# Performance work log

Hardware: AMD Instinct MI355X
Metric: run time of the kernel (lower is better)

Reference implementation:

```python
import jax, jax.numpy as jnp
import numpy as np

N, H, HEADS, E = 4096, 256, 4, 262144
DH = H // HEADS
EPS = 1e-5


def _ln(x, g, b):
    mu = jnp.mean(x, axis=-1, keepdims=True)
    var = jnp.mean(jnp.square(x - mu), axis=-1, keepdims=True)
    return (x - mu) / jnp.sqrt(var + EPS) * g + b


def setup_inputs() -> dict:
    key = jax.random.key(0)
    ks = jax.random.split(key, 20)
    s = 0.02
    inp = {
        "h": jax.random.normal(ks[0], (N, H), jnp.float32),
        "edge_index": jax.random.randint(ks[1], (2, E), 0, N, jnp.int64 if jax.config.read("jax_enable_x64") else jnp.int32),
        "W_src": jax.random.normal(ks[2], (H, H), jnp.float32) * s,
        "b_src": jnp.zeros((H,), jnp.float32),
        "W_tgt": jax.random.normal(ks[3], (H, H), jnp.float32) * s,
        "b_tgt": jnp.zeros((H,), jnp.float32),
        "Wq": jax.random.normal(ks[4], (H, H), jnp.float32) * s,
        "bq": jnp.zeros((H,), jnp.float32),
        "Wk": jax.random.normal(ks[5], (H, H), jnp.float32) * s,
        "bk": jnp.zeros((H,), jnp.float32),
        "Wv": jax.random.normal(ks[6], (H, H), jnp.float32) * s,
        "bv": jnp.zeros((H,), jnp.float32),
        "Wo": jax.random.normal(ks[7], (H, H), jnp.float32) * s,
        "bo": jnp.zeros((H,), jnp.float32),
        "W1": jax.random.normal(ks[8], (H, 2 * H), jnp.float32) * s,
        "b1": jnp.zeros((2 * H,), jnp.float32),
        "W2": jax.random.normal(ks[9], (2 * H, H), jnp.float32) * s,
        "b2": jnp.zeros((H,), jnp.float32),
        "g1": jnp.ones((H,), jnp.float32),
        "be1": jnp.zeros((H,), jnp.float32),
        "g2": jnp.ones((H,), jnp.float32),
        "be2": jnp.zeros((H,), jnp.float32),
    }
    return inp


def reference(h, edge_index, W_src, b_src, W_tgt, b_tgt, Wq, bq, Wk, bk, Wv, bv,
              Wo, bo, W1, b1, W2, b2, g1, be1, g2, be2):
    src, dst = edge_index[0], edge_index[1]
    # gather + linear + add per edge: (E, H)
    edge_emb = (h[src] @ W_src + b_src) + (h[dst] @ W_tgt + b_tgt)
    # scatter-add to target nodes, normalize by in-degree (clamped at 1)
    agg = jax.ops.segment_sum(edge_emb, dst, num_segments=N)
    deg = jax.ops.segment_sum(jnp.ones((E,), h.dtype), dst, num_segments=N)
    agg = agg / jnp.maximum(deg, 1.0)[:, None]
    # multi-head attention: queries = h, keys/values = agg (batch=1, seq=N)
    q = (h @ Wq + bq).reshape(N, HEADS, DH)
    k = (agg @ Wk + bk).reshape(N, HEADS, DH)
    v = (agg @ Wv + bv).reshape(N, HEADS, DH)
    scores = jnp.einsum("nhd,mhd->hnm", q, k) / jnp.sqrt(jnp.asarray(DH, h.dtype))
    attn = jax.nn.softmax(scores, axis=-1)
    ctx = jnp.einsum("hnm,mhd->nhd", attn, v).reshape(N, H)
    attn_out = ctx @ Wo + bo
    # residual + LN (dropout is identity in eval mode)
    x = _ln(h + attn_out, g1, be1)
    ffn = jax.nn.gelu(x @ W1 + b1, approximate=False) @ W2 + b2
    return _ln(x + ffn, g2, be2)
```

## Files before the change

### kernel.cpp

```cpp
#include <hip/hip_runtime.h>

#define N_NODES 4096
#define HID 256
#define N_EDGES 262144
#define N_HEADS 4
#define DHEAD 64

typedef unsigned short u16;
typedef unsigned long long u64;
typedef __attribute__((ext_vector_type(8))) short bf16x8;
typedef __attribute__((ext_vector_type(4))) float f32x4;

__device__ __forceinline__ float b2f(u16 u) {
  union { unsigned int i; float f; } c; c.i = ((unsigned int)u) << 16; return c.f;
}
__device__ __forceinline__ u16 f2b(float f) {
  union { float f; unsigned int i; } c; c.f = f;
  unsigned int x = c.i;
  unsigned int r = (x + 0x7fffu + ((x >> 16) & 1u)) >> 16;
  return (u16)r;
}
__device__ __forceinline__ u16 f2b_trunc(float f) {
  union { float f; unsigned int i; } c; c.f = f;
  return (u16)(c.i >> 16);
}

struct PrepArgs {
  const void* wsrc[8]; u16* wdst[8]; int wR[8]; int wC[8]; int wboff[8];
  const void* bs[12]; u16* bd[12]; int bn[12];
};
__global__ __launch_bounds__(256) void k_prep(
    const void* __restrict__ h_r, u16* __restrict__ h_c, PrepArgs P,
    const unsigned* __restrict__ g1raw, const unsigned* __restrict__ eiraw,
    const int* __restrict__ ei, int* __restrict__ cnt, int* __restrict__ flags) {
  __shared__ u16 t[32][33];
  int b = blockIdx.x, tid = threadIdx.x;
  int f = (g1raw[0] == 0x3F800000u) ? 1 : 0;
  if (b < 1024) {
    int gi = b * 256 + tid;
    if (f) {
      float4 v = ((const float4*)h_r)[gi];
      u64 pk = (u64)f2b(v.x) | ((u64)f2b(v.y) << 16) |
               ((u64)f2b(v.z) << 32) | ((u64)f2b(v.w) << 48);
      ((u64*)h_c)[gi] = pk;
    } else {
      ((uint2*)h_c)[gi] = ((const uint2*)h_r)[gi];
    }
  } else if (b < 1664) {
    int rb = b - 1024;
    int jj = 0;
#pragma unroll
    for (int i2 = 1; i2 < 8; i2++) jj = (rb >= P.wboff[i2]) ? i2 : jj;
    int local = rb - P.wboff[jj];
    int C = P.wC[jj], R = P.wR[jj];
    int nbx = C / 32;
    int c0 = (local % nbx) * 32, r0 = (local / nbx) * 32;
    int tx = tid & 31, ty = tid >> 5;
    const void* src = P.wsrc[jj];
    u16* dst = P.wdst[jj];
    for (int i = ty; i < 32; i += 8) {
      size_t idx = (size_t)(r0 + i) * C + c0 + tx;
      t[i][tx] = f ? f2b(((const float*)src)[idx]) : ((const u16*)src)[idx];
    }
    __syncthreads();
    for (int i = ty; i < 32; i += 8)
      dst[(size_t)(c0 + i) * R + r0 + tx] = t[tx][i];
  } else if (b == 1664) {
    if (tid == 0) {
      unsigned any = 0;
      for (int i = 0; i < 64; i++) any |= eiraw[2 * i + 1];
      flags[0] = f;
      flags[1] = (any == 0u) ? 1 : 0;
    }
    for (int j = 0; j < 12; j++)
      for (int i = tid; i < P.bn[j]; i += 256)
        P.bd[j][i] = f ? f2b(((const float*)P.bs[j])[i]) : ((const u16*)P.bs[j])[i];
  } else {
    unsigned hi = eiraw[2 * (tid & 63) + 1];
#pragma unroll
    for (int m2 = 1; m2 <= 32; m2 <<= 1) hi |= __shfl_xor(hi, m2, 64);
    int i64 = (hi == 0u);
    int e = (b - 1665) * 256 + tid;
    int d = i64 ? ei[2 * (N_EDGES + e)] : ei[N_EDGES + e];
    atomicAdd(&cnt[d], 1);
  }
}

__global__ void k_scan(const int* __restrict__ cnt, int* __restrict__ row_start,
                       int* __restrict__ cursor) {
  __shared__ int part[256];
  int t = threadIdx.x;
  int loc[16];
  int s = 0;
#pragma unroll
  for (int i = 0; i < 16; i++) { loc[i] = s; s += cnt[t * 16 + i]; }
  part[t] = s;
  __syncthreads();
  for (int ofs = 1; ofs < 256; ofs <<= 1) {
    int v = (t >= ofs) ? part[t - ofs] : 0;
    __syncthreads();
    part[t] += v;
    __syncthreads();
  }
  int excl = part[t] - s;
#pragma unroll
  for (int i = 0; i < 16; i++) {
    int v = excl + loc[i];
    row_start[t * 16 + i] = v;
    cursor[t * 16 + i] = v;
  }
  if (t == 255) row_start[N_NODES] = part[255];
}

__global__ void k_fill(const int* __restrict__ ei, int* __restrict__ cursor,
                       int* __restrict__ eidx, const unsigned* __restrict__ eiraw) {
  int tid = threadIdx.x;
  unsigned hi = eiraw[2 * (tid & 63) + 1];
#pragma unroll
  for (int m2 = 1; m2 <= 32; m2 <<= 1) hi |= __shfl_xor(hi, m2, 64);
  int i64 = (hi == 0u);
  int e = blockIdx.x * 256 + tid;
  int d = i64 ? ei[2 * (N_EDGES + e)] : ei[N_EDGES + e];
  int s = i64 ? ei[2 * e] : ei[e];
  int pos = atomicAdd(&cursor[d], 1);
  eidx[pos] = s;
}

__global__ __launch_bounds__(256) void k_gather(
    const int* __restrict__ row_start, const int* __restrict__ eidx,
    const u16* __restrict__ hs, const u16* __restrict__ ht,
    u16* __restrict__ aggb) {
  int n = blockIdx.x, t = threadIdx.x;
  int beg = row_start[n], end = row_start[n + 1];
  float acc = 0.f;
  int j = beg;
  for (; j + 3 < end; j += 4) {
    int s0 = eidx[j], s1 = eidx[j + 1], s2 = eidx[j + 2], s3 = eidx[j + 3];
    acc += b2f(hs[(size_t)s0 * HID + t]);
    acc += b2f(hs[(size_t)s1 * HID + t]);
    acc += b2f(hs[(size_t)s2 * HID + t]);
    acc += b2f(hs[(size_t)s3 * HID + t]);
  }
  for (; j < end; j++) acc += b2f(hs[(size_t)eidx[j] * HID + t]);
  float dg = (float)(end - beg);
  float a = (acc + dg * b2f(ht[(size_t)n * HID + t])) / fmaxf(dg, 1.f);
  aggb[(size_t)n * HID + t] = f2b(a);
}

struct GemmOuts { void* p[3]; int mode[3]; float scale[3]; };
template <int GELU>
__global__ __launch_bounds__(256) void k_gemm_bt(
    const u16* __restrict__ A, const u16* __restrict__ Bt,
    const u16* __restrict__ bias, GemmOuts outs, int ncol, int K) {
  __shared__ u16 As[64][72];
  __shared__ u16 Bs[64][72];
  int tid = threadIdx.x;
  int wave = tid >> 6, lane = tid & 63;
  int ln = lane & 15, quad = lane >> 4;
  int m0 = blockIdx.y * 64, n0 = blockIdx.x * 64;
  int wm = (wave >> 1) * 32, wn = (wave & 1) * 32;
  int srow = tid >> 2, scol = (tid & 3) * 16;
  const u16* pA = &A[(size_t)(m0 + srow) * K + scol];
  const u16* pB = &Bt[(size_t)(n0 + srow) * K + scol];
  f32x4 acc[2][2] = {};
  for (int k0 = 0; k0 < K; k0 += 64) {
    uint4 va0 = *(const uint4*)(pA + k0);
    uint4 va1 = *(const uint4*)(pA + k0 + 8);
    uint4 vb0 = *(const uint4*)(pB + k0);
    uint4 vb1 = *(const uint4*)(pB + k0 + 8);
    __syncthreads();
    *(uint4*)&As[srow][scol] = va0; *(uint4*)&As[srow][scol + 8] = va1;
    *(uint4*)&Bs[srow][scol] = vb0; *(uint4*)&Bs[srow][scol + 8] = vb1;
    __syncthreads();
#pragma unroll
    for (int s2 = 0; s2 < 2; s2++) {
      bf16x8 a0 = *(const bf16x8*)&As[wm + ln][s2 * 32 + quad * 8];
      bf16x8 a1 = *(const bf16x8*)&As[wm + 16 + ln][s2 * 32 + quad * 8];
      bf16x8 b0 = *(const bf16x8*)&Bs[wn + ln][s2 * 32 + quad * 8];
      bf16x8 b1 = *(const bf16x8*)&Bs[wn + 16 + ln][s2 * 32 + quad * 8];
      acc[0][0] = __builtin_amdgcn_mfma_f32_16x16x32_bf16(a0, b0, acc[0][0], 0, 0, 0);
      acc[0][1] = __builtin_amdgcn_mfma_f32_16x16x32_bf16(a0, b1, acc[0][1], 0, 0, 0);
      acc[1][0] = __builtin_amdgcn_mfma_f32_16x16x32_bf16(a1, b0, acc[1][0], 0, 0, 0);
      acc[1][1] = __builtin_amdgcn_mfma_f32_16x16x32_bf16(a1, b1, acc[1][1], 0, 0, 0);
    }
  }
  int which = n0 / ncol;
  int nloc0 = n0 - which * ncol;
  int md = outs.mode[which];
  float sc = outs.scale[which];
#pragma unroll
  for (int t = 0; t < 2; t++)
#pragma unroll
    for (int u = 0; u < 2; u++) {
      int lc = nloc0 + wn + u * 16 + ln;
      float bb = b2f(bias[n0 + wn + u * 16 + ln]);
      float c4[4];
#pragma unroll
      for (int r = 0; r < 4; r++) {
        float c = (acc[t][u][r] + bb) * sc;
        if (GELU) c = 0.5f * c * (1.0f + erff(c * 0.70710678118654752f));
        c4[r] = c;
      }
      int gm0 = m0 + wm + t * 16 + quad * 4;
      if (md == 0) {
        u16* dp = (u16*)outs.p[which];
#pragma unroll
        for (int r = 0; r < 4; r++) dp[(size_t)(gm0 + r) * ncol + lc] = f2b(c4[r]);
      } else if (md == 1) {
        float* dp = (float*)outs.p[which];
#pragma unroll
        for (int r = 0; r < 4; r++) dp[(size_t)(gm0 + r) * ncol + lc] = c4[r];
      } else {
        u64 pk = (u64)f2b(c4[0]) | ((u64)f2b(c4[1]) << 16) |
                 ((u64)f2b(c4[2]) << 32) | ((u64)f2b(c4[3]) << 48);
        *(u64*)&((u16*)outs.p[which])[(size_t)lc * 4096 + gm0] = pk;
      }
    }
}

struct PoPtrs { u16* p[8]; };
struct PoCPtrs { const u16* p[8]; };
__global__ __launch_bounds__(256) void k_attn_split(
    const u16* __restrict__ q, const u16* __restrict__ k,
    const u16* __restrict__ vt, PoPtrs pw, float* __restrict__ lout, int S) {
  __shared__ u16 ks[64][72];
  __shared__ u16 vs[64][72];
  __shared__ u16 ps[4][16][72];
  int tid = threadIdx.x;
  int wv = tid >> 6, lane = tid & 63, ln = lane & 15, quad = lane >> 4;
  int hh = blockIdx.y, q0 = blockIdx.x * 64, bz = blockIdx.z;
  int kchunk = N_NODES / S;
  int kbeg = bz * kchunk, kend = kbeg + kchunk;
  const u16* qrow = &q[(size_t)(q0 + wv * 16 + ln) * HID + hh * DHEAD];
  bf16x8 aq0 = *(const bf16x8*)&qrow[quad * 8];
  bf16x8 aq1 = *(const bf16x8*)&qrow[32 + quad * 8];
  f32x4 o[4] = {};
  float l_r[4] = {0.f, 0.f, 0.f, 0.f};
  int srow = tid >> 2, scol = (tid & 3) * 16;
  const u16* kbase = &k[(size_t)srow * HID + hh * DHEAD + scol];
  const u16* vbase = &vt[(size_t)(hh * DHEAD + srow) * N_NODES + scol];

  for (int k0 = kbeg; k0 < kend; k0 += 64) {
    *(uint4*)&ks[srow][scol]     = *(const uint4*)(kbase + (size_t)k0 * HID);
    *(uint4*)&ks[srow][scol + 8] = *(const uint4*)(kbase + (size_t)k0 * HID + 8);
    *(uint4*)&vs[srow][scol]     = *(const uint4*)(vbase + k0);
    *(uint4*)&vs[srow][scol + 8] = *(const uint4*)(vbase + k0 + 8);
    __syncthreads();

    f32x4 s[4];
#pragma unroll
    for (int u = 0; u < 4; u++) {
      bf16x8 b0 = *(const bf16x8*)&ks[u * 16 + ln][quad * 8];
      bf16x8 b1 = *(const bf16x8*)&ks[u * 16 + ln][32 + quad * 8];
      f32x4 z = {};
      z = __builtin_amdgcn_mfma_f32_16x16x32_bf16(aq0, b0, z, 0, 0, 0);
      s[u] = __builtin_amdgcn_mfma_f32_16x16x32_bf16(aq1, b1, z, 0, 0, 0);
    }
#pragma unroll
    for (int u = 0; u < 4; u++)
#pragma unroll
      for (int r = 0; r < 4; r++) {
        float p = __expf(s[u][r]);
        l_r[r] += p;
        ps[wv][quad * 4 + r][u * 16 + ln] = f2b_trunc(p);
      }
    __syncthreads();

    bf16x8 ap0 = *(const bf16x8*)&ps[wv][ln][quad * 8];
    bf16x8 ap1 = *(const bf16x8*)&ps[wv][ln][32 + quad * 8];
#pragma unroll
    for (int u = 0; u < 4; u++) {
      bf16x8 bv0 = *(const bf16x8*)&vs[u * 16 + ln][quad * 8];
      bf16x8 bv1 = *(const bf16x8*)&vs[u * 16 + ln][32 + quad * 8];
      o[u] = __builtin_amdgcn_mfma_f32_16x16x32_bf16(ap0, bv0, o[u], 0, 0, 0);
      o[u] = __builtin_amdgcn_mfma_f32_16x16x32_bf16(ap1, bv1, o[u], 0, 0, 0);
    }
    __syncthreads();
  }
  u16* po = pw.p[bz];
#pragma unroll
  for (int u = 0; u < 4; u++)
#pragma unroll
    for (int r = 0; r < 4; r++) {
      int row = q0 + wv * 16 + quad * 4 + r;
      po[((size_t)hh * N_NODES + row) * DHEAD + u * 16 + ln] = f2b(o[u][r]);
    }
#pragma unroll
  for (int mask = 1; mask <= 8; mask <<= 1)
#pragma unroll
    for (int r = 0; r < 4; r++) l_r[r] += __shfl_xor(l_r[r], mask, 64);
  if (ln == 0) {
#pragma unroll
    for (int r = 0; r < 4; r++) {
      int row = q0 + wv * 16 + quad * 4 + r;
      lout[(size_t)(bz * N_HEADS + hh) * N_NODES + row] = l_r[r];
    }
  }
}

__global__ __launch_bounds__(256) void k_attn_combine(
    PoCPtrs pp, const float* __restrict__ lsum, u16* __restrict__ ctx, int S) {
  int t = threadIdx.x;
  int d = t & 63, qq = t >> 6;
  int qrow = blockIdx.x * 4 + qq;
  for (int h = 0; h < N_HEADS; h++) {
    float L = 0.f, o = 0.f;
    for (int s = 0; s < S; s++) {
      L += lsum[(size_t)(s * N_HEADS + h) * N_NODES + qrow];
      o += b2f(pp.p[s][((size_t)h * N_NODES + qrow) * DHEAD + d]);
    }
    ctx[(size_t)qrow * HID + h * DHEAD + d] = f2b(o / L);
  }
}

template <int FINAL>
__global__ __launch_bounds__(256) void k_ln(
    const u16* __restrict__ a, const float* __restrict__ b,
    const u16* __restrict__ g, const u16* __restrict__ be,
    void* __restrict__ out, const int* __restrict__ flags) {
  int tid = threadIdx.x, wv = tid >> 6, lane = tid & 63;
  int row = blockIdx.x * 4 + wv;
  size_t base = (size_t)row * HID + lane * 4;
  uint2 av = *(const uint2*)&a[base];
  float4 bv4 = *(const float4*)&b[base];
  float v[4];
  v[0] = b2f((u16)(av.x & 0xffff)) + bv4.x;
  v[1] = b2f((u16)(av.x >> 16)) + bv4.y;
  v[2] = b2f((u16)(av.y & 0xffff)) + bv4.z;
  v[3] = b2f((u16)(av.y >> 16)) + bv4.w;
  float sum = v[0] + v[1] + v[2] + v[3];
#pragma unroll
  for (int mask = 1; mask <= 32; mask <<= 1) sum += __shfl_xor(sum, mask, 64);
  float mu = sum * (1.0f / HID);
  float d[4], sq = 0.f;
#pragma unroll
  for (int i = 0; i < 4; i++) { d[i] = v[i] - mu; sq += d[i] * d[i]; }
#pragma unroll
  for (int mask = 1; mask <= 32; mask <<= 1) sq += __shfl_xor(sq, mask, 64);
  float rstd = rsqrtf(sq * (1.0f / HID) + 1e-5f);
  uint2 gv = *(const uint2*)&g[lane * 4];
  uint2 bev = *(const uint2*)&be[lane * 4];
  float res[4];
  res[0] = d[0] * rstd * b2f((u16)(gv.x & 0xffff)) + b2f((u16)(bev.x & 0xffff));
  res[1] = d[1] * rstd * b2f((u16)(gv.x >> 16)) + b2f((u16)(bev.x >> 16));
  res[2] = d[2] * rstd * b2f((u16)(gv.y & 0xffff)) + b2f((u16)(bev.y & 0xffff));
  res[3] = d[3] * rstd * b2f((u16)(gv.y >> 16)) + b2f((u16)(bev.y >> 16));
#pragma unroll
  for (int i = 0; i < 4; i++)
    if (!(fabsf(res[i]) < 1e30f)) res[i] = FINAL ? 1000.0f : 300.0f;
  if (FINAL && flags[0]) {
    *(float4*)&((float*)out)[base] = make_float4(res[0], res[1], res[2], res[3]);
  } else {
    u64 pk = (u64)f2b(res[0]) | ((u64)f2b(res[1]) << 16) |
             ((u64)f2b(res[2]) << 32) | ((u64)f2b(res[3]) << 48);
    *(u64*)&((u16*)out)[base] = pk;
  }
}

extern "C" void kernel_launch(void* const* d_in, const int* in_sizes, int n_in,
                              void* d_out, int out_size, void* d_ws, size_t ws_size,
                              hipStream_t stream) {
  (void)in_sizes; (void)n_in; (void)out_size;
  const void* h_r    = d_in[0];
  const int*  ei     = (const int*)d_in[1];
  const void* W_r[8] = {d_in[2], d_in[4], d_in[6], d_in[8], d_in[10], d_in[12], d_in[14], d_in[16]};
  const void* b_r[12] = {d_in[3], d_in[5], d_in[7], d_in[9], d_in[11], d_in[13],
                         d_in[15], d_in[17], d_in[18], d_in[19], d_in[20], d_in[21]};

  char* w = (char*)d_ws;
  const size_t MB = 1024 * 1024;
  u16* bufA = (u16*)(w + 0 * MB);
  u16* bufC = (u16*)(w + 2 * MB);
  u16* bufE = (u16*)(w + 4 * MB);
  u16* bufF = (u16*)(w + 6 * MB);
  u16* bufB = (u16*)(w + 8 * MB);
  u16* bufD = (u16*)(w + 10 * MB);
  u16* h_c  = (u16*)(w + 12 * MB);
  size_t off = 14 * MB;
  auto alloc = [&](size_t bytes) -> void* {
    void* p = (void*)(w + off);
    off += (bytes + 255) & ~(size_t)255;
    return p;
  };
  u16* WsrcT = (u16*)alloc((size_t)HID * HID * 2);
  u16* WtgtT = (u16*)alloc((size_t)HID * HID * 2);
  u16* WqT   = (u16*)alloc((size_t)HID * HID * 2);
  u16* WkT   = (u16*)alloc((size_t)HID * HID * 2);
  u16* WvT   = (u16*)alloc((size_t)HID * HID * 2);
  u16* WoT   = (u16*)alloc((size_t)HID * HID * 2);
  u16* W1T   = (u16*)alloc((size_t)HID * 2 * HID * 2);
  u16* W2T   = (u16*)alloc((size_t)HID * 2 * HID * 2);
  u16* bsrc = (u16*)alloc(512); u16* btgt = (u16*)alloc(512);
  u16* bq   = (u16*)alloc(512); u16* bk   = (u16*)alloc(512);
  u16* bv   = (u16*)alloc(512); u16* bo   = (u16*)alloc(512);
  u16* b1   = (u16*)alloc(1024); u16* b2  = (u16*)alloc(512);
  u16* g1   = (u16*)alloc(512); u16* be1  = (u16*)alloc(512);
  u16* g2   = (u16*)alloc(512); u16* be2  = (u16*)alloc(512);
  int* flags = (int*)alloc(256);
  int* cnt  = (int*)alloc((size_t)N_NODES * 4);
  int* rsrt = (int*)alloc((size_t)(N_NODES + 1) * 4);
  int* cur  = (int*)alloc((size_t)N_NODES * 4);
  int* eidx = (int*)alloc((size_t)N_EDGES * 4);

  u16* hs = bufA;  u16* ht = bufB;  u16* qb = bufC;
  u16* aggb = bufD; u16* kb = bufE; u16* vt = bufB;
  u16* ctxb = bufA; u16* xb = bufD;
  float* attn_out = (float*)bufE;
  u16* ffn1 = bufE;
  float* yf = (float*)bufA;
  float* lsum = (float*)eidx;

  int S = 2;
  PoPtrs pw{}; PoCPtrs pc{};
  pw.p[0] = bufF; pw.p[1] = bufD;
  if (ws_size >= off + 12 * MB + 64) {
    S = 8;
    for (int i = 2; i < 8; i++) pw.p[i] = (u16*)(w + off + (size_t)(i - 2) * 2 * MB);
  } else if (ws_size >= off + 4 * MB + 64) {
    S = 4;
    pw.p[2] = (u16*)(w + off);
    pw.p[3] = (u16*)(w + off + 2 * MB);
  }
  for (int i = 0; i < 8; i++) pc.p[i] = pw.p[i];

  hipMemsetAsync(cnt, 0, (size_t)N_NODES * 4, stream);
  PrepArgs P;
  u16* Wdsts[8] = {WsrcT, WtgtT, WqT, WkT, WvT, WoT, W1T, W2T};
  int WR[8] = {HID, HID, HID, HID, HID, HID, HID, 2 * HID};
  int WC[8] = {HID, HID, HID, HID, HID, HID, 2 * HID, HID};
  int boff = 0;
  for (int i = 0; i < 8; i++) {
    P.wsrc[i] = W_r[i]; P.wdst[i] = Wdsts[i]; P.wR[i] = WR[i]; P.wC[i] = WC[i];
    P.wboff[i] = boff;
    boff += (WR[i] / 32) * (WC[i] / 32);
  }
  u16* bdsts[12] = {bsrc, btgt, bq, bk, bv, bo, b1, b2, g1, be1, g2, be2};
  int bns[12] = {256, 256, 256, 256, 256, 256, 512, 256, 256, 256, 256, 256};
  for (int i = 0; i < 12; i++) { P.bs[i] = b_r[i]; P.bd[i] = bdsts[i]; P.bn[i] = bns[i]; }
  k_prep<<<2689, 256, 0, stream>>>(h_r, h_c, P, (const unsigned*)d_in[18],
                                   (const unsigned*)ei, ei, cnt, flags);
  k_scan<<<1, 256, 0, stream>>>(cnt, rsrt, cur);
  k_fill<<<N_EDGES / 256, 256, 0, stream>>>(ei, cur, eidx, (const unsigned*)ei);

  {
    GemmOuts go;
    go.p[0] = hs; go.p[1] = ht; go.p[2] = qb;
    go.mode[0] = 0; go.mode[1] = 0; go.mode[2] = 0;
    go.scale[0] = 1.f; go.scale[1] = 1.f; go.scale[2] = 0.125f;
    k_gemm_bt<0><<<dim3(12, 64), 256, 0, stream>>>(h_c, WsrcT, bsrc, go, HID, HID);
  }
  k_gather<<<N_NODES, 256, 0, stream>>>(rsrt, eidx, hs, ht, aggb);

  {
    GemmOuts go;
    go.p[0] = kb; go.p[1] = vt; go.p[2] = nullptr;
    go.mode[0] = 0; go.mode[1] = 2; go.mode[2] = 0;
    go.scale[0] = 1.f; go.scale[1] = 1.f; go.scale[2] = 1.f;
    k_gemm_bt<0><<<dim3(8, 64), 256, 0, stream>>>(aggb, WkT, bk, go, HID, HID);
  }

  k_attn_split<<<dim3(N_NODES / 64, N_HEADS, S), 256, 0, stream>>>(qb, kb, vt, pw, lsum, S);
  k_attn_combine<<<N_NODES / 4, 256, 0, stream>>>(pc, lsum, ctxb, S);

  {
    GemmOuts go;
    go.p[0] = attn_out; go.p[1] = nullptr; go.p[2] = nullptr;
    go.mode[0] = 1; go.mode[1] = 0; go.mode[2] = 0;
    go.scale[0] = 1.f; go.scale[1] = 1.f; go.scale[2] = 1.f;
    k_gemm_bt<0><<<dim3(4, 64), 256, 0, stream>>>(ctxb, WoT, bo, go, HID, HID);
  }
  k_ln<0><<<N_NODES / 4, 256, 0, stream>>>(h_c, attn_out, g1, be1, xb, flags);

  {
    GemmOuts go;
    go.p[0] = ffn1; go.p[1] = nullptr; go.p[2] = nullptr;
    go.mode[0] = 0; go.mode[1] = 0; go.mode[2] = 0;
    go.scale[0] = 1.f; go.scale[1] = 1.f; go.scale[2] = 1.f;
    k_gemm_bt<1><<<dim3(8, 64), 256, 0, stream>>>(xb, W1T, b1, go, 2 * HID, HID);
  }
  {
    GemmOuts go;
    go.p[0] = yf; go.p[1] = nullptr; go.p[2] = nullptr;
    go.mode[0] = 1; go.mode[1] = 0; go.mode[2] = 0;
    go.scale[0] = 1.f; go.scale[1] = 1.f; go.scale[2] = 1.f;
    k_gemm_bt<0><<<dim3(4, 64), 256, 0, stream>>>(ffn1, W2T, b2, go, HID, 2 * HID);
  }
  k_ln<1><<<N_NODES / 4, 256, 0, stream>>>(xb, yf, g2, be2, d_out, flags);
}
```

Before: 257.6 us.

## Drop LDS staging in GEMMs and software-pipeline attention with MFMA row sums

The GEMM kernel now loads MFMA operands straight from global memory with a compile-time K and unrolled loop, removing the LDS staging and its barriers. The split attention kernel prefetches the next K/V tile into registers while computing the current one. It computes softmax row sums with an MFMA against a ones vector instead of scalar accumulation and shuffles. It also swaps __expf for exp2 by folding log2(e) into the Q scale. The risks are that direct global loads lose reuse across waves and depend on cache hits, and that the row sum is now taken over bf16-truncated probabilities.

```diff
diff --git a/kernel.cpp b/kernel.cpp
--- a/kernel.cpp
+++ b/kernel.cpp
@@ -148,52 +148,42 @@
 }
 
 struct GemmOuts { void* p[3]; int mode[3]; float scale[3]; };
-template <int GELU>
-__global__ __launch_bounds__(256) void k_gemm_bt(
+template <int GELU, int K>
+__global__ __launch_bounds__(256) void k_gemm_nl(
     const u16* __restrict__ A, const u16* __restrict__ Bt,
-    const u16* __restrict__ bias, GemmOuts outs, int ncol, int K) {
-  __shared__ u16 As[64][72];
-  __shared__ u16 Bs[64][72];
+    const u16* __restrict__ bias, GemmOuts outs, int ncol) {
   int tid = threadIdx.x;
   int wave = tid >> 6, lane = tid & 63;
   int ln = lane & 15, quad = lane >> 4;
-  int m0 = blockIdx.y * 64, n0 = blockIdx.x * 64;
-  int wm = (wave >> 1) * 32, wn = (wave & 1) * 32;
-  int srow = tid >> 2, scol = (tid & 3) * 16;
-  const u16* pA = &A[(size_t)(m0 + srow) * K + scol];
-  const u16* pB = &Bt[(size_t)(n0 + srow) * K + scol];
+  int m0 = blockIdx.y * 64 + (wave >> 1) * 32;
+  int n0 = blockIdx.x * 64 + (wave & 1) * 32;
+  const u16* pA0 = &A[(size_t)(m0 + ln) * K + quad * 8];
+  const u16* pA1 = &A[(size_t)(m0 + 16 + ln) * K + quad * 8];
+  const u16* pB0 = &Bt[(size_t)(n0 + ln) * K + quad * 8];
+  const u16* pB1 = &Bt[(size_t)(n0 + 16 + ln) * K + quad * 8];
   f32x4 acc[2][2] = {};
-  for (int k0 = 0; k0 < K; k0 += 64) {
-    uint4 va0 = *(const uint4*)(pA + k0);
-    uint4 va1 = *(const uint4*)(pA + k0 + 8);
-    uint4 vb0 = *(const uint4*)(pB + k0);
-    uint4 vb1 = *(const uint4*)(pB + k0 + 8);
-    __syncthreads();
-    *(uint4*)&As[srow][scol] = va0; *(uint4*)&As[srow][scol + 8] = va1;
-    *(uint4*)&Bs[srow][scol] = vb0; *(uint4*)&Bs[srow][scol + 8] = vb1;
-    __syncthreads();
-#pragma unroll
-    for (int s2 = 0; s2 < 2; s2++) {
-      bf16x8 a0 = *(const bf16x8*)&As[wm + ln][s2 * 32 + quad * 8];
-      bf16x8 a1 = *(const bf16x8*)&As[wm + 16 + ln][s2 * 32 + quad * 8];
-      bf16x8 b0 = *(const bf16x8*)&Bs[wn + ln][s2 * 32 + quad * 8];
-      bf16x8 b1 = *(const bf16x8*)&Bs[wn + 16 + ln][s2 * 32 + quad * 8];
-      acc[0][0] = __builtin_amdgcn_mfma_f32_16x16x32_bf16(a0, b0, acc[0][0], 0, 0, 0);
-      acc[0][1] = __builtin_amdgcn_mfma_f32_16x16x32_bf16(a0, b1, acc[0][1], 0, 0, 0);
-      acc[1][0] = __builtin_amdgcn_mfma_f32_16x16x32_bf16(a1, b0, acc[1][0], 0, 0, 0);
-      acc[1][1] = __builtin_amdgcn_mfma_f32_16x16x32_bf16(a1, b1, acc[1][1], 0, 0, 0);
-    }
-  }
-  int which = n0 / ncol;
-  int nloc0 = n0 - which * ncol;
+#pragma unroll 4
+  for (int k0 = 0; k0 < K; k0 += 32) {
+    bf16x8 a0 = *(const bf16x8*)(pA0 + k0);
+    bf16x8 a1 = *(const bf16x8*)(pA1 + k0);
+    bf16x8 b0 = *(const bf16x8*)(pB0 + k0);
+    bf16x8 b1 = *(const bf16x8*)(pB1 + k0);
+    acc[0][0] = __builtin_amdgcn_mfma_f32_16x16x32_bf16(a0, b0, acc[0][0], 0, 0, 0);
+    acc[0][1] = __builtin_amdgcn_mfma_f32_16x16x32_bf16(a0, b1, acc[0][1], 0, 0, 0);
+    acc[1][0] = __builtin_amdgcn_mfma_f32_16x16x32_bf16(a1, b0, acc[1][0], 0, 0, 0);
+    acc[1][1] = __builtin_amdgcn_mfma_f32_16x16x32_bf16(a1, b1, acc[1][1], 0, 0, 0);
+  }
+  int nblk = blockIdx.x * 64;
+  int which = nblk / ncol;
   int md = outs.mode[which];
   float sc = outs.scale[which];
 #pragma unroll
   for (int t = 0; t < 2; t++)
 #pragma unroll
     for (int u = 0; u < 2; u++) {
-      int lc = nloc0 + wn + u * 16 + ln;
-      float bb = b2f(bias[n0 + wn + u * 16 + ln]);
+      int gn = n0 + u * 16 + ln;
+      int lc = gn - which * ncol;
+      float bb = b2f(bias[gn]);
       float c4[4];
 #pragma unroll
       for (int r = 0; r < 4; r++) {
@@ -201,7 +191,7 @@
         if (GELU) c = 0.5f * c * (1.0f + erff(c * 0.70710678118654752f));
         c4[r] = c;
       }
-      int gm0 = m0 + wm + t * 16 + quad * 4;
+      int gm0 = m0 + t * 16 + quad * 4;
       if (md == 0) {
         u16* dp = (u16*)outs.p[which];
 #pragma unroll
@@ -234,19 +224,30 @@
   const u16* qrow = &q[(size_t)(q0 + wv * 16 + ln) * HID + hh * DHEAD];
   bf16x8 aq0 = *(const bf16x8*)&qrow[quad * 8];
   bf16x8 aq1 = *(const bf16x8*)&qrow[32 + quad * 8];
+  bf16x8 ones;
+#pragma unroll
+  for (int i = 0; i < 8; i++) ones[i] = (short)0x3F80;
   f32x4 o[4] = {};
-  float l_r[4] = {0.f, 0.f, 0.f, 0.f};
+  f32x4 ol = {};
   int srow = tid >> 2, scol = (tid & 3) * 16;
   const u16* kbase = &k[(size_t)srow * HID + hh * DHEAD + scol];
   const u16* vbase = &vt[(size_t)(hh * DHEAD + srow) * N_NODES + scol];
 
+  *(uint4*)&ks[srow][scol]     = *(const uint4*)(kbase + (size_t)kbeg * HID);
+  *(uint4*)&ks[srow][scol + 8] = *(const uint4*)(kbase + (size_t)kbeg * HID + 8);
+  *(uint4*)&vs[srow][scol]     = *(const uint4*)(vbase + kbeg);
+  *(uint4*)&vs[srow][scol + 8] = *(const uint4*)(vbase + kbeg + 8);
+  __syncthreads();
+
   for (int k0 = kbeg; k0 < kend; k0 += 64) {
-    *(uint4*)&ks[srow][scol]     = *(const uint4*)(kbase + (size_t)k0 * HID);
-    *(uint4*)&ks[srow][scol + 8] = *(const uint4*)(kbase + (size_t)k0 * HID + 8);
-    *(uint4*)&vs[srow][scol]     = *(const uint4*)(vbase + k0);
-    *(uint4*)&vs[srow][scol + 8] = *(const uint4*)(vbase + k0 + 8);
-    __syncthreads();
-
+    bool more = (k0 + 64 < kend);
+    uint4 ka0, ka1, va0, va1;
+    if (more) {
+      ka0 = *(const uint4*)(kbase + (size_t)(k0 + 64) * HID);
+      ka1 = *(const uint4*)(kbase + (size_t)(k0 + 64) * HID + 8);
+      va0 = *(const uint4*)(vbase + k0 + 64);
+      va1 = *(const uint4*)(vbase + k0 + 72);
+    }
     f32x4 s[4];
 #pragma unroll
     for (int u = 0; u < 4; u++) {
@@ -259,13 +260,11 @@
 #pragma unroll
     for (int u = 0; u < 4; u++)
 #pragma unroll
-      for (int r = 0; r < 4; r++) {
-        float p = __expf(s[u][r]);
-        l_r[r] += p;
-        ps[wv][quad * 4 + r][u * 16 + ln] = f2b_trunc(p);
-      }
-    __syncthreads();
-
+      for (int r = 0; r < 4; r++)
+        ps[wv][quad * 4 + r][u * 16 + ln] = f2b_trunc(__builtin_amdgcn_exp2f(s[u][r]));
+    __builtin_amdgcn_sched_barrier(0);
+    __builtin_amdgcn_s_waitcnt(0xC07F);
+    __builtin_amdgcn_sched_barrier(0);
     bf16x8 ap0 = *(const bf16x8*)&ps[wv][ln][quad * 8];
     bf16x8 ap1 = *(const bf16x8*)&ps[wv][ln][32 + quad * 8];
 #pragma unroll
@@ -275,6 +274,15 @@
       o[u] = __builtin_amdgcn_mfma_f32_16x16x32_bf16(ap0, bv0, o[u], 0, 0, 0);
       o[u] = __builtin_amdgcn_mfma_f32_16x16x32_bf16(ap1, bv1, o[u], 0, 0, 0);
     }
+    ol = __builtin_amdgcn_mfma_f32_16x16x32_bf16(ap0, ones, ol, 0, 0, 0);
+    ol = __builtin_amdgcn_mfma_f32_16x16x32_bf16(ap1, ones, ol, 0, 0, 0);
+    __syncthreads();
+    if (more) {
+      *(uint4*)&ks[srow][scol]     = ka0;
+      *(uint4*)&ks[srow][scol + 8] = ka1;
+      *(uint4*)&vs[srow][scol]     = va0;
+      *(uint4*)&vs[srow][scol + 8] = va1;
+    }
     __syncthreads();
   }
   u16* po = pw.p[bz];
@@ -285,15 +293,11 @@
       int row = q0 + wv * 16 + quad * 4 + r;
       po[((size_t)hh * N_NODES + row) * DHEAD + u * 16 + ln] = f2b(o[u][r]);
     }
-#pragma unroll
-  for (int mask = 1; mask <= 8; mask <<= 1)
-#pragma unroll
-    for (int r = 0; r < 4; r++) l_r[r] += __shfl_xor(l_r[r], mask, 64);
   if (ln == 0) {
 #pragma unroll
     for (int r = 0; r < 4; r++) {
       int row = q0 + wv * 16 + quad * 4 + r;
-      lout[(size_t)(bz * N_HEADS + hh) * N_NODES + row] = l_r[r];
+      lout[(size_t)(bz * N_HEADS + hh) * N_NODES + row] = ol[r];
     }
   }
 }
@@ -446,8 +450,8 @@
     GemmOuts go;
     go.p[0] = hs; go.p[1] = ht; go.p[2] = qb;
     go.mode[0] = 0; go.mode[1] = 0; go.mode[2] = 0;
-    go.scale[0] = 1.f; go.scale[1] = 1.f; go.scale[2] = 0.125f;
-    k_gemm_bt<0><<<dim3(12, 64), 256, 0, stream>>>(h_c, WsrcT, bsrc, go, HID, HID);
+    go.scale[0] = 1.f; go.scale[1] = 1.f; go.scale[2] = 0.180336880f;
+    k_gemm_nl<0, 256><<<dim3(12, 64), 256, 0, stream>>>(h_c, WsrcT, bsrc, go, HID);
   }
   k_gather<<<N_NODES, 256, 0, stream>>>(rsrt, eidx, hs, ht, aggb);
 
@@ -456,7 +460,7 @@
     go.p[0] = kb; go.p[1] = vt; go.p[2] = nullptr;
     go.mode[0] = 0; go.mode[1] = 2; go.mode[2] = 0;
     go.scale[0] = 1.f; go.scale[1] = 1.f; go.scale[2] = 1.f;
-    k_gemm_bt<0><<<dim3(8, 64), 256, 0, stream>>>(aggb, WkT, bk, go, HID, HID);
+    k_gemm_nl<0, 256><<<dim3(8, 64), 256, 0, stream>>>(aggb, WkT, bk, go, HID);
   }
 
   k_attn_split<<<dim3(N_NODES / 64, N_HEADS, S), 256, 0, stream>>>(qb, kb, vt, pw, lsum, S);
@@ -467,7 +471,7 @@
     go.p[0] = attn_out; go.p[1] = nullptr; go.p[2] = nullptr;
     go.mode[0] = 1; go.mode[1] = 0; go.mode[2] = 0;
     go.scale[0] = 1.f; go.scale[1] = 1.f; go.scale[2] = 1.f;
-    k_gemm_bt<0><<<dim3(4, 64), 256, 0, stream>>>(ctxb, WoT, bo, go, HID, HID);
+    k_gemm_nl<0, 256><<<dim3(4, 64), 256, 0, stream>>>(ctxb, WoT, bo, go, HID);
   }
   k_ln<0><<<N_NODES / 4, 256, 0, stream>>>(h_c, attn_out, g1, be1, xb, flags);
 
@@ -476,14 +480,14 @@
     go.p[0] = ffn1; go.p[1] = nullptr; go.p[2] = nullptr;
     go.mode[0] = 0; go.mode[1] = 0; go.mode[2] = 0;
     go.scale[0] = 1.f; go.scale[1] = 1.f; go.scale[2] = 1.f;
-    k_gemm_bt<1><<<dim3(8, 64), 256, 0, stream>>>(xb, W1T, b1, go, 2 * HID, HID);
+    k_gemm_nl<1, 256><<<dim3(8, 64), 256, 0, stream>>>(xb, W1T, b1, go, 2 * HID);
   }
   {
     GemmOuts go;
     go.p[0] = yf; go.p[1] = nullptr; go.p[2] = nullptr;
     go.mode[0] = 1; go.mode[1] = 0; go.mode[2] = 0;
     go.scale[0] = 1.f; go.scale[1] = 1.f; go.scale[2] = 1.f;
-    k_gemm_bt<0><<<dim3(4, 64), 256, 0, stream>>>(ffn1, W2T, b2, go, HID, 2 * HID);
+    k_gemm_nl<0, 512><<<dim3(4, 64), 256, 0, stream>>>(ffn1, W2T, b2, go, HID);
   }
   k_ln<1><<<N_NODES / 4, 256, 0, stream>>>(xb, yf, g2, be2, d_out, flags);
 }
```

Result: slower. 275.8 us (+7.1%).

## Prefetch next K/V tile in registers, use exp2 and MFMA row sums

Applied to the files above, without the earlier changes.

The attention split kernel now loads the next K/V tile into registers while the current tile is being computed, which overlaps global load latency with MFMA work. The softmax exponent becomes a native exp2, with log2(e) folded into the Q scale, so the separate multiply in expf goes away. Row sums of P are computed by an MFMA against a ones vector instead of per-lane adds plus a shuffle reduction, and the P sum now uses the bf16-truncated values. One barrier is removed inside the wave-private P section, but an extra barrier is added before the shared-memory store, and register pressure rises from the prefetch buffers.

```diff
diff --git a/kernel.cpp b/kernel.cpp
--- a/kernel.cpp
+++ b/kernel.cpp
@@ -234,19 +234,30 @@
   const u16* qrow = &q[(size_t)(q0 + wv * 16 + ln) * HID + hh * DHEAD];
   bf16x8 aq0 = *(const bf16x8*)&qrow[quad * 8];
   bf16x8 aq1 = *(const bf16x8*)&qrow[32 + quad * 8];
+  bf16x8 ones;
+#pragma unroll
+  for (int i = 0; i < 8; i++) ones[i] = (short)0x3F80;
   f32x4 o[4] = {};
-  float l_r[4] = {0.f, 0.f, 0.f, 0.f};
+  f32x4 ol = {};
   int srow = tid >> 2, scol = (tid & 3) * 16;
   const u16* kbase = &k[(size_t)srow * HID + hh * DHEAD + scol];
   const u16* vbase = &vt[(size_t)(hh * DHEAD + srow) * N_NODES + scol];
 
+  *(uint4*)&ks[srow][scol]     = *(const uint4*)(kbase + (size_t)kbeg * HID);
+  *(uint4*)&ks[srow][scol + 8] = *(const uint4*)(kbase + (size_t)kbeg * HID + 8);
+  *(uint4*)&vs[srow][scol]     = *(const uint4*)(vbase + kbeg);
+  *(uint4*)&vs[srow][scol + 8] = *(const uint4*)(vbase + kbeg + 8);
+  __syncthreads();
+
   for (int k0 = kbeg; k0 < kend; k0 += 64) {
-    *(uint4*)&ks[srow][scol]     = *(const uint4*)(kbase + (size_t)k0 * HID);
-    *(uint4*)&ks[srow][scol + 8] = *(const uint4*)(kbase + (size_t)k0 * HID + 8);
-    *(uint4*)&vs[srow][scol]     = *(const uint4*)(vbase + k0);
-    *(uint4*)&vs[srow][scol + 8] = *(const uint4*)(vbase + k0 + 8);
-    __syncthreads();
-
+    bool more = (k0 + 64 < kend);
+    uint4 ka0, ka1, va0, va1;
+    if (more) {
+      ka0 = *(const uint4*)(kbase + (size_t)(k0 + 64) * HID);
+      ka1 = *(const uint4*)(kbase + (size_t)(k0 + 64) * HID + 8);
+      va0 = *(const uint4*)(vbase + k0 + 64);
+      va1 = *(const uint4*)(vbase + k0 + 72);
+    }
     f32x4 s[4];
 #pragma unroll
     for (int u = 0; u < 4; u++) {
@@ -259,13 +270,8 @@
 #pragma unroll
     for (int u = 0; u < 4; u++)
 #pragma unroll
-      for (int r = 0; r < 4; r++) {
-        float p = __expf(s[u][r]);
-        l_r[r] += p;
-        ps[wv][quad * 4 + r][u * 16 + ln] = f2b_trunc(p);
-      }
-    __syncthreads();
-
+      for (int r = 0; r < 4; r++)
+        ps[wv][quad * 4 + r][u * 16 + ln] = f2b_trunc(__builtin_amdgcn_exp2f(s[u][r]));
     bf16x8 ap0 = *(const bf16x8*)&ps[wv][ln][quad * 8];
     bf16x8 ap1 = *(const bf16x8*)&ps[wv][ln][32 + quad * 8];
 #pragma unroll
@@ -275,6 +281,15 @@
       o[u] = __builtin_amdgcn_mfma_f32_16x16x32_bf16(ap0, bv0, o[u], 0, 0, 0);
       o[u] = __builtin_amdgcn_mfma_f32_16x16x32_bf16(ap1, bv1, o[u], 0, 0, 0);
     }
+    ol = __builtin_amdgcn_mfma_f32_16x16x32_bf16(ap0, ones, ol, 0, 0, 0);
+    ol = __builtin_amdgcn_mfma_f32_16x16x32_bf16(ap1, ones, ol, 0, 0, 0);
+    __syncthreads();
+    if (more) {
+      *(uint4*)&ks[srow][scol]     = ka0;
+      *(uint4*)&ks[srow][scol + 8] = ka1;
+      *(uint4*)&vs[srow][scol]     = va0;
+      *(uint4*)&vs[srow][scol + 8] = va1;
+    }
     __syncthreads();
   }
   u16* po = pw.p[bz];
@@ -285,15 +300,11 @@
       int row = q0 + wv * 16 + quad * 4 + r;
       po[((size_t)hh * N_NODES + row) * DHEAD + u * 16 + ln] = f2b(o[u][r]);
     }
-#pragma unroll
-  for (int mask = 1; mask <= 8; mask <<= 1)
-#pragma unroll
-    for (int r = 0; r < 4; r++) l_r[r] += __shfl_xor(l_r[r], mask, 64);
   if (ln == 0) {
 #pragma unroll
     for (int r = 0; r < 4; r++) {
       int row = q0 + wv * 16 + quad * 4 + r;
-      lout[(size_t)(bz * N_HEADS + hh) * N_NODES + row] = l_r[r];
+      lout[(size_t)(bz * N_HEADS + hh) * N_NODES + row] = ol[r];
     }
   }
 }
@@ -446,7 +457,7 @@
     GemmOuts go;
     go.p[0] = hs; go.p[1] = ht; go.p[2] = qb;
     go.mode[0] = 0; go.mode[1] = 0; go.mode[2] = 0;
-    go.scale[0] = 1.f; go.scale[1] = 1.f; go.scale[2] = 0.125f;
+    go.scale[0] = 1.f; go.scale[1] = 1.f; go.scale[2] = 0.180336880f;
     k_gemm_bt<0><<<dim3(12, 64), 256, 0, stream>>>(h_c, WsrcT, bsrc, go, HID, HID);
   }
   k_gather<<<N_NODES, 256, 0, stream>>>(rsrt, eidx, hs, ht, aggb);
```

Result: no change. 253.7 us (-1.5%).
